# Performance work log

Measured on AMD Instinct MI355X. Metric: run time of the kernel, lower is better.

## Reference

```python
import jax, jax.numpy as jnp
import numpy as np

NC, L, C, V, H = 4, 3, 32, 512, 512
B, T, N = 32, 64, 8

def setup_inputs() -> dict:
    key = jax.random.key(0)
    ks = jax.random.split(key, 12)
    inp = {
        "x": jax.random.normal(ks[0], (B, T, N, H), dtype=jnp.float32),
        "comms": jax.random.randint(ks[1], (B, T, N, NC, L), 0, V, dtype=jnp.int64),
        "codebook": jax.random.normal(ks[2], (L, V, C), dtype=jnp.float32),
    }
    for l in range(L):
        fan_in = H + l * NC * C
        inp[f"W{l}"] = jax.random.normal(ks[3 + 2 * l], (NC * V, fan_in), dtype=jnp.float32) / np.sqrt(fan_in)
        inp[f"b{l}"] = jax.random.normal(ks[4 + 2 * l], (NC * V,), dtype=jnp.float32) * 0.01
    return inp


def reference(x, comms, codebook, W0, b0, W1, b1, W2, b2):
    # x: [B,T,N,H]; comms: [B,T,N,NC,L] int indices; codebook: [L,V,C]
    Bs, Ts, Ns, _ = x.shape
    params = [(W0, b0), (W1, b1), (W2, b2)]
    cond = x
    log_probs = jnp.zeros((Bs, Ts, Ns), dtype=x.dtype)
    entropy = jnp.zeros((Bs, Ts, Ns), dtype=x.dtype)
    hard_levels, soft_levels = [], []
    for l in range(L):
        W, b = params[l]
        logits = (cond @ W.T + b).reshape(Bs, Ts, Ns, NC, V)
        logp = jax.nn.log_softmax(logits, axis=-1)
        p = jnp.exp(logp)
        idx = comms[..., l]  # [B,T,N,NC]
        # log-prob of chosen codes, summed over comm channels
        lp = jnp.take_along_axis(logp, idx[..., None], axis=-1)[..., 0]
        log_probs = log_probs + lp.sum(axis=-1)
        # categorical entropy, summed over comm channels
        entropy = entropy + (-(p * logp).sum(axis=-1)).sum(axis=-1)
        hard = codebook[l][idx]                               # [B,T,N,NC,C]
        soft = jnp.einsum('btnkv,vc->btnkc', p, codebook[l])  # [B,T,N,NC,C]
        hard_levels.append(hard)
        soft_levels.append(soft)
        cond = jnp.concatenate([cond, hard.reshape(Bs, Ts, Ns, NC * C)], axis=-1)
    hard_s = jnp.stack(hard_levels, axis=-2)  # [B,T,N,NC,L,C]
    soft_s = jnp.stack(soft_levels, axis=-2)
    # straight-through estimator
    codewords = soft_s + jax.lax.stop_gradient(hard_s - soft_s)
    comm_output = codewords.sum(axis=-2).reshape(-1, NC * C)  # sum over hq levels
    return comm_output, log_probs, entropy
```

## Files before the change

kernel.cpp:

```cpp
#include <hip/hip_runtime.h>
#include <hip/hip_bf16.h>

#define NCC 4
#define LL 3
#define CCC 32
#define VVV 512
#define HHH 512
#define ROWS_TOTAL 16384
#define CONDW 768

typedef float f32x4 __attribute__((ext_vector_type(4)));
typedef long  i64x2 __attribute__((ext_vector_type(2)));

__device__ __forceinline__ void gload_lds16(const void* g, void* l) {
    __builtin_amdgcn_global_load_lds(
        (const __attribute__((address_space(1))) void*)g,
        (__attribute__((address_space(3))) void*)l, 16, 0, 0);
}

__device__ __forceinline__ int pk4_fp8(float a, float b, float c, float d) {
    int w = __builtin_amdgcn_cvt_pk_fp8_f32(a, b, 0, false);
    w = __builtin_amdgcn_cvt_pk_fp8_f32(c, d, w, true);
    return w;
}

__device__ __forceinline__ int perm_off(int b) {
    return (b & ~63) | ((b & 0x18) << 1) | ((b & 0x20) >> 2) | (b & 7);
}

__global__ void convert_w_pack(const float* __restrict__ src, unsigned char* __restrict__ dst, int K) {
    const int j  = blockIdx.x * 256 + threadIdx.x;
    const int kc = K >> 3;
    const int r  = j / kc;
    const int k0 = (j - r * kc) * 8;
    const float4 v0 = *reinterpret_cast<const float4*>(src + (size_t)r * K + k0);
    const float4 v1 = *reinterpret_cast<const float4*>(src + (size_t)r * K + k0 + 4);
    int2 p;
    p.x = pk4_fp8(v0.x, v0.y, v0.z, v0.w);
    p.y = pk4_fp8(v1.x, v1.y, v1.z, v1.w);
    const int ct = r >> 4, lc = r & 15;
    const int t = k0 >> 6, s = (k0 >> 5) & 1, kq = (k0 >> 3) & 3;
    const size_t off = ((size_t)((t * 128 + ct) * 64 + kq * 16 + lc)) * 16 + s * 8;
    *reinterpret_cast<int2*>(dst + off) = p;
}

__global__ void build_cond(const float* __restrict__ x,
                           const int* __restrict__ comms,
                           const float* __restrict__ codebook,
                           unsigned char* __restrict__ cond,
                           float* __restrict__ comm_out) {
    const int r = blockIdx.x;
    const int t = threadIdx.x;
    const float4 v = reinterpret_cast<const float4*>(x + (size_t)r * HHH)[t];
    unsigned char* crow = cond + (size_t)r * CONDW;
    *reinterpret_cast<int*>(crow + perm_off(t * 4)) = pk4_fp8(v.x, v.y, v.z, v.w);
    const int k = t >> 5, c = t & 31;
    float s = 0.f;
    #pragma unroll
    for (int l = 0; l < LL; ++l) {
        const int vi = comms[r * (NCC * LL) + k * LL + l];
        const float val = codebook[((size_t)(l * VVV + vi)) * CCC + c];
        s += val;
        if (l < 2)
            crow[perm_off(HHH + l * (NCC * CCC) + t)] =
                (unsigned char)(__builtin_amdgcn_cvt_pk_fp8_f32(val, val, 0, false) & 0xff);
    }
    comm_out[(size_t)r * (NCC * CCC) + t] = s;
}

__global__ __launch_bounds__(256, 4) void gemm_partials(
    const unsigned char* __restrict__ cond,
    const unsigned char* __restrict__ wq,
    const float* __restrict__ b0, const float* __restrict__ b1, const float* __restrict__ b2,
    const int* __restrict__ comms,
    float4* __restrict__ partials)
{
    const int rb  = blockIdx.x;
    const int y   = blockIdx.y;
    const int lvl = blockIdx.z;
    const int K = HHH + lvl * (NCC * CCC);
    const unsigned char* Wp =
        wq + (lvl == 0 ? 0 : (lvl == 1 ? 2048 * 512 : 2048 * 512 + 2048 * 640));
    const float* bias = (lvl == 0) ? b0 : (lvl == 1 ? b1 : b2);

    const int tid  = threadIdx.x;
    const int lane = tid & 63;
    const int w    = tid >> 6;
    const int wr   = w >> 1;
    const int wc   = w & 1;
    const int lc   = lane & 15;
    const int kq   = lane >> 4;
    const int rchunk = (kq ^ ((lc >> 1) & 3)) << 4;

    const int rowBase = rb * 128;

    __shared__ __align__(16) char LDS[16384];

    const int sc = (lane & 3) ^ ((lane >> 3) & 3);
    const unsigned char* gA = cond + (size_t)(rowBase + w * 32 + (lane >> 2)) * CONDW + sc * 16;
    const unsigned char* gBf = Wp + ((size_t)(y * 8 + wc * 4) * 64 + lane) * 16;

#define STAGE_A(B, KS) do {                                            \
        char* ab = LDS + (B) * 8192 + w * 2048;                        \
        gload_lds16(gA + (KS), ab);                                    \
        gload_lds16(gA + (size_t)16 * CONDW + (KS), ab + 1024);        \
    } while (0)

    f32x4 acc[4][4] = {};

    const int NT = K >> 6;
    STAGE_A(0, 0);
    asm volatile("s_waitcnt vmcnt(0)" ::: "memory");
    __builtin_amdgcn_s_barrier();

    for (int t = 0; t < NT; ++t) {
        const int cur = t & 1;
        i64x2 bf[4];
        #pragma unroll
        for (int n = 0; n < 4; ++n)
            bf[n] = *reinterpret_cast<const i64x2*>(gBf + (size_t)t * 131072 + n * 1024);
        if (t + 1 < NT) STAGE_A(cur ^ 1, (t + 1) * 64);
        const char* Ab = LDS + cur * 8192;
        i64x2 af[4];
        #pragma unroll
        for (int m = 0; m < 4; ++m)
            af[m] = *reinterpret_cast<const i64x2*>(
                Ab + (wr * 64 + m * 16 + lc) * 64 + rchunk);
        __builtin_amdgcn_s_setprio(1);
        #pragma unroll
        for (int m = 0; m < 4; ++m)
            #pragma unroll
            for (int n = 0; n < 4; ++n)
                acc[m][n] = __builtin_amdgcn_mfma_f32_16x16x32_fp8_fp8(
                    af[m][0], bf[n][0], acc[m][n], 0, 0, 0);
        #pragma unroll
        for (int m = 0; m < 4; ++m)
            #pragma unroll
            for (int n = 0; n < 4; ++n)
                acc[m][n] = __builtin_amdgcn_mfma_f32_16x16x32_fp8_fp8(
                    af[m][1], bf[n][1], acc[m][n], 0, 0, 0);
        __builtin_amdgcn_s_setprio(0);
        asm volatile("s_waitcnt vmcnt(0)" ::: "memory");
        __builtin_amdgcn_s_barrier();
    }
#undef STAGE_A

    float* redS  = (float*)LDS;
    float* redT  = redS + 256;
    float* redTL = redT + 256;

    const int g   = y >> 2;
    const int cig = y & 3;
    const int colBase = y * 128;
    float bv[4];
    #pragma unroll
    for (int n = 0; n < 4; ++n) bv[n] = bias[colBase + wc * 64 + n * 16 + lc];

    #pragma unroll
    for (int m = 0; m < 4; ++m) {
        float sv[4] = {0, 0, 0, 0}, tv[4] = {0, 0, 0, 0};
        #pragma unroll
        for (int i = 0; i < 4; ++i) {
            #pragma unroll
            for (int n = 0; n < 4; ++n) {
                const float z = acc[m][n][i] + bv[n];
                const float e = __expf(z);
                sv[i] += e;
                tv[i] += e * z;
            }
            #pragma unroll
            for (int off = 1; off < 16; off <<= 1) {
                sv[i] += __shfl_xor(sv[i], off);
                tv[i] += __shfl_xor(tv[i], off);
            }
        }
        #pragma unroll
        for (int i = 0; i < 4; ++i) {
            const int rloc = wr * 64 + m * 16 + kq * 4 + i;
            const int tcol = comms[(size_t)(rowBase + rloc) * (NCC * LL) + g * LL + lvl];
            #pragma unroll
            for (int n = 0; n < 4; ++n) {
                const int colg = cig * 128 + wc * 64 + n * 16 + lc;
                if (colg == tcol) redTL[rloc] = acc[m][n][i] + bv[n];
            }
        }
        if (lc == 0) {
            #pragma unroll
            for (int i = 0; i < 4; ++i) {
                const int rloc = wr * 64 + m * 16 + kq * 4 + i;
                redS[wc * 128 + rloc] = sv[i];
                redT[wc * 128 + rloc] = tv[i];
            }
        }
    }
    __syncthreads();
    if (tid < 128) {
        const int r = tid;
        const float S = redS[r] + redS[128 + r];
        const float T = redT[r] + redT[128 + r];
        partials[((size_t)lvl * ROWS_TOTAL + rowBase + r) * 16 + y] =
            make_float4(0.f, S, T, redTL[r]);
    }
}

__global__ void combine(const float4* __restrict__ partials,
                        const int* __restrict__ comms,
                        float* __restrict__ lp_out, float* __restrict__ ent_out)
{
    const int row = blockIdx.x * 256 + threadIdx.x;
    if (row >= ROWS_TOTAL) return;
    float lp = 0.f, ent = 0.f;
    #pragma unroll
    for (int lvl = 0; lvl < LL; ++lvl) {
        const float4* base = partials + ((size_t)lvl * ROWS_TOTAL + row) * 16;
        #pragma unroll
        for (int g = 0; g < NCC; ++g) {
            const int tcol = comms[(size_t)row * (NCC * LL) + g * LL + lvl];
            float S = 0.f, T = 0.f, tl = 0.f;
            #pragma unroll
            for (int k = 0; k < 4; ++k) {
                const float4 c = base[g * 4 + k];
                S += c.y;
                T += c.z;
                if ((tcol >> 7) == k) tl = c.w;
            }
            const float logZ = __logf(S);
            ent += logZ - T / S;
            lp += tl - logZ;
        }
    }
    lp_out[row] = lp;
    ent_out[row] = ent;
}

extern "C" void kernel_launch(void* const* d_in, const int* in_sizes, int n_in,
                              void* d_out, int out_size, void* d_ws, size_t ws_size,
                              hipStream_t stream) {
    const float* x        = (const float*)d_in[0];
    const int*   comms    = (const int*)d_in[1];
    const float* codebook = (const float*)d_in[2];
    const float* W0 = (const float*)d_in[3];
    const float* b0 = (const float*)d_in[4];
    const float* W1 = (const float*)d_in[5];
    const float* b1 = (const float*)d_in[6];
    const float* W2 = (const float*)d_in[7];
    const float* b2 = (const float*)d_in[8];

    float* out      = (float*)d_out;
    float* comm_out = out;
    float* lp_out   = out + (size_t)ROWS_TOTAL * 128;
    float* ent_out  = lp_out + ROWS_TOTAL;

    unsigned char* wq   = (unsigned char*)d_ws;
    unsigned char* cond = (unsigned char*)d_ws + 7864320;
    float4*       parts = (float4*)((char*)d_ws + 7864320 + 12582912);

    const int n0 = 2048 * 512, n1 = 2048 * 640, n2 = 2048 * 768;
    convert_w_pack<<<512, 256, 0, stream>>>(W0, wq, 512);
    convert_w_pack<<<640, 256, 0, stream>>>(W1, wq + n0, 640);
    convert_w_pack<<<768, 256, 0, stream>>>(W2, wq + n0 + n1, 768);

    build_cond<<<ROWS_TOTAL, 128, 0, stream>>>(x, comms, codebook, cond, comm_out);

    dim3 grid(ROWS_TOTAL / 128, 16, LL);
    gemm_partials<<<grid, 256, 0, stream>>>(cond, wq, b0, b1, b2, comms, parts);

    combine<<<ROWS_TOTAL / 256, 256, 0, stream>>>(parts, comms, lp_out, ent_out);
}
```

Baseline: 145.8 us.

## Switch FP8 GEMM to 16x16x128 scaled MFMA with 128-wide K tiles

Replaces the 16x16x32 fp8 MFMA with the gfx950 scaled 16x16x128 f8f6f4 MFMA, using unit scales (0x7f exponent). The K tile per iteration doubles to 128, so the weight packing, the cond row permutation, the LDS staging layout and swizzle, and the LDS buffer size (now 32KB) all change to match. The goal is fewer MFMA issues and fewer loop iterations and barriers. In exchange, LDS use per block doubles, which may reduce occupancy, and register pressure rises from the 8-dword operands.

```diff
diff --git a/kernel.cpp b/kernel.cpp
--- a/kernel.cpp
+++ b/kernel.cpp
@@ -10,7 +10,8 @@
 #define CONDW 768
 
 typedef float f32x4 __attribute__((ext_vector_type(4)));
-typedef long  i64x2 __attribute__((ext_vector_type(2)));
+typedef int   i32x4 __attribute__((ext_vector_type(4)));
+typedef int   i32x8 __attribute__((ext_vector_type(8)));
 
 __device__ __forceinline__ void gload_lds16(const void* g, void* l) {
     __builtin_amdgcn_global_load_lds(
@@ -24,8 +25,8 @@
     return w;
 }
 
-__device__ __forceinline__ int perm_off(int b) {
-    return (b & ~63) | ((b & 0x18) << 1) | ((b & 0x20) >> 2) | (b & 7);
+__device__ __forceinline__ int perm128(int b) {
+    return (b & ~0x70) | ((b & 0x10) << 2) | ((b & 0x60) >> 1);
 }
 
 __global__ void convert_w_pack(const float* __restrict__ src, unsigned char* __restrict__ dst, int K) {
@@ -39,8 +40,8 @@
     p.x = pk4_fp8(v0.x, v0.y, v0.z, v0.w);
     p.y = pk4_fp8(v1.x, v1.y, v1.z, v1.w);
     const int ct = r >> 4, lc = r & 15;
-    const int t = k0 >> 6, s = (k0 >> 5) & 1, kq = (k0 >> 3) & 3;
-    const size_t off = ((size_t)((t * 128 + ct) * 64 + kq * 16 + lc)) * 16 + s * 8;
+    const int t = k0 >> 7, kq = (k0 >> 5) & 3, j0 = k0 & 31;
+    const size_t off = ((size_t)((t * 128 + ct) * 64 + kq * 16 + lc)) * 32 + j0;
     *reinterpret_cast<int2*>(dst + off) = p;
 }
 
@@ -53,7 +54,7 @@
     const int t = threadIdx.x;
     const float4 v = reinterpret_cast<const float4*>(x + (size_t)r * HHH)[t];
     unsigned char* crow = cond + (size_t)r * CONDW;
-    *reinterpret_cast<int*>(crow + perm_off(t * 4)) = pk4_fp8(v.x, v.y, v.z, v.w);
+    *reinterpret_cast<int*>(crow + perm128(t * 4)) = pk4_fp8(v.x, v.y, v.z, v.w);
     const int k = t >> 5, c = t & 31;
     float s = 0.f;
     #pragma unroll
@@ -62,7 +63,7 @@
         const float val = codebook[((size_t)(l * VVV + vi)) * CCC + c];
         s += val;
         if (l < 2)
-            crow[perm_off(HHH + l * (NCC * CCC) + t)] =
+            crow[perm128(HHH + l * (NCC * CCC) + t)] =
                 (unsigned char)(__builtin_amdgcn_cvt_pk_fp8_f32(val, val, 0, false) & 0xff);
     }
     comm_out[(size_t)r * (NCC * CCC) + t] = s;
@@ -90,55 +91,59 @@
     const int wc   = w & 1;
     const int lc   = lane & 15;
     const int kq   = lane >> 4;
-    const int rchunk = (kq ^ ((lc >> 1) & 3)) << 4;
+    const int l7   = lc & 7;
+    const int c0   = (kq ^ l7) << 4;
+    const int c1   = ((4 + kq) ^ l7) << 4;
 
     const int rowBase = rb * 128;
 
-    __shared__ __align__(16) char LDS[16384];
-
-    const int sc = (lane & 3) ^ ((lane >> 3) & 3);
-    const unsigned char* gA = cond + (size_t)(rowBase + w * 32 + (lane >> 2)) * CONDW + sc * 16;
-    const unsigned char* gBf = Wp + ((size_t)(y * 8 + wc * 4) * 64 + lane) * 16;
-
-#define STAGE_A(B, KS) do {                                            \
-        char* ab = LDS + (B) * 8192 + w * 2048;                        \
-        gload_lds16(gA + (KS), ab);                                    \
-        gload_lds16(gA + (size_t)16 * CONDW + (KS), ab + 1024);        \
+    __shared__ __align__(16) char LDS[32768];
+
+    const int sr = lane >> 3;
+    const int sc = (lane & 7) ^ sr;
+    const unsigned char* gA = cond + (size_t)(rowBase + w * 8 + sr) * CONDW + sc * 16;
+    const unsigned char* gBf = Wp + ((size_t)(y * 8 + wc * 4) * 64 + lane) * 32;
+
+#define STAGE_A(B, KS) do {                                                  \
+        char* ab = LDS + (B) * 16384 + w * 1024;                             \
+        _Pragma("unroll")                                                    \
+        for (int j = 0; j < 4; ++j)                                          \
+            gload_lds16(gA + (size_t)(j * 32) * CONDW + (KS), ab + j * 4096);\
     } while (0)
 
     f32x4 acc[4][4] = {};
 
-    const int NT = K >> 6;
+    const int NT = K >> 7;
     STAGE_A(0, 0);
     asm volatile("s_waitcnt vmcnt(0)" ::: "memory");
     __builtin_amdgcn_s_barrier();
 
     for (int t = 0; t < NT; ++t) {
         const int cur = t & 1;
-        i64x2 bf[4];
-        #pragma unroll
-        for (int n = 0; n < 4; ++n)
-            bf[n] = *reinterpret_cast<const i64x2*>(gBf + (size_t)t * 131072 + n * 1024);
-        if (t + 1 < NT) STAGE_A(cur ^ 1, (t + 1) * 64);
-        const char* Ab = LDS + cur * 8192;
-        i64x2 af[4];
-        #pragma unroll
-        for (int m = 0; m < 4; ++m)
-            af[m] = *reinterpret_cast<const i64x2*>(
-                Ab + (wr * 64 + m * 16 + lc) * 64 + rchunk);
+        i32x8 bf[4];
+        #pragma unroll
+        for (int n = 0; n < 4; ++n) {
+            const i32x4 lo = *reinterpret_cast<const i32x4*>(
+                gBf + (size_t)t * 262144 + n * 2048);
+            const i32x4 hi = *reinterpret_cast<const i32x4*>(
+                gBf + (size_t)t * 262144 + n * 2048 + 16);
+            bf[n] = __builtin_shufflevector(lo, hi, 0, 1, 2, 3, 4, 5, 6, 7);
+        }
+        if (t + 1 < NT) STAGE_A(cur ^ 1, (t + 1) * 128);
+        const char* Ab = LDS + cur * 16384;
         __builtin_amdgcn_s_setprio(1);
         #pragma unroll
-        for (int m = 0; m < 4; ++m)
+        for (int m = 0; m < 4; ++m) {
+            const int ro = (wr * 64 + m * 16 + lc) * 128;
+            const i32x4 alo = *reinterpret_cast<const i32x4*>(Ab + ro + c0);
+            const i32x4 ahi = *reinterpret_cast<const i32x4*>(Ab + ro + c1);
+            const i32x8 af = __builtin_shufflevector(alo, ahi, 0, 1, 2, 3, 4, 5, 6, 7);
             #pragma unroll
             for (int n = 0; n < 4; ++n)
-                acc[m][n] = __builtin_amdgcn_mfma_f32_16x16x32_fp8_fp8(
-                    af[m][0], bf[n][0], acc[m][n], 0, 0, 0);
-        #pragma unroll
-        for (int m = 0; m < 4; ++m)
-            #pragma unroll
-            for (int n = 0; n < 4; ++n)
-                acc[m][n] = __builtin_amdgcn_mfma_f32_16x16x32_fp8_fp8(
-                    af[m][1], bf[n][1], acc[m][n], 0, 0, 0);
+                acc[m][n] = __builtin_amdgcn_mfma_scale_f32_16x16x128_f8f6f4(
+                    af, bf[n], acc[m][n], 0, 0,
+                    0, 0x7f7f7f7f, 0, 0x7f7f7f7f);
+        }
         __builtin_amdgcn_s_setprio(0);
         asm volatile("s_waitcnt vmcnt(0)" ::: "memory");
         __builtin_amdgcn_s_barrier();
```

After: 128.2 us. -12.1%, faster.
